# Kernel tuning notes

Hardware: AMD Instinct MI355X
Metric: run time of the kernel (lower is better)

## Reference

```python
import jax, jax.numpy as jnp
import numpy as np

N_NODES = 100000
N_EDGES = 3200000
N_FEAT = 64
HID = 64
GDIM = 32
N_CLASS = 2
NUM_GRAPHS = 16


def setup_inputs() -> dict:
    key = jax.random.key(0)
    ks = jax.random.split(key, 24)

    def w(k, fan_in, fan_out):
        return (jax.random.normal(k, (fan_in, fan_out), jnp.float32) / np.sqrt(fan_in)).astype(jnp.float32)

    inp = {
        'x': jax.random.normal(ks[0], (N_NODES, N_FEAT), jnp.float32),
        'edge_index': jax.random.randint(ks[1], (2, N_EDGES), 0, N_NODES, jnp.int32),
        'batch': jnp.sort(jax.random.randint(ks[2], (N_NODES,), 0, NUM_GRAPHS, jnp.int32)),
        # lin0: nr_features -> nhid0
        'lin0_w': w(ks[3], N_FEAT, HID), 'lin0_b': jnp.zeros((HID,), jnp.float32),
        # SAGEConv 1: lin_l (aggregated, with bias), lin_r (self, no bias)
        's1_lw': w(ks[4], HID, HID), 's1_lb': jnp.zeros((HID,), jnp.float32), 's1_rw': w(ks[5], HID, HID),
        # SAGEConv 2
        's2_lw': w(ks[6], HID, HID), 's2_lb': jnp.zeros((HID,), jnp.float32), 's2_rw': w(ks[7], HID, HID),
        # embedding heads
        'emb0_w': w(ks[8], HID, GDIM), 'emb0_b': jnp.zeros((GDIM,), jnp.float32),
        'emb1_w': w(ks[9], HID, GDIM), 'emb1_b': jnp.zeros((GDIM,), jnp.float32),
        'emb2_w': w(ks[10], HID, GDIM), 'emb2_b': jnp.zeros((GDIM,), jnp.float32),
        'merge_w': w(ks[11], 3 * GDIM, GDIM), 'merge_b': jnp.zeros((GDIM,), jnp.float32),
        # global attention pooling: gate_nn (GDIM->1), v_nn (GDIM->GDIM)
        'gate_w': w(ks[12], GDIM, 1), 'gate_b': jnp.zeros((1,), jnp.float32),
        'v_w': w(ks[13], GDIM, GDIM), 'v_b': jnp.zeros((GDIM,), jnp.float32),
        'out_w': w(ks[14], GDIM, N_CLASS), 'out_b': jnp.zeros((N_CLASS,), jnp.float32),
    }
    return inp


def _sage(x, src, dst, lw, lb, rw):
    # mean aggregation of source features at destination nodes
    deg = jax.ops.segment_sum(jnp.ones_like(src, jnp.float32), dst, num_segments=N_NODES)
    agg = jax.ops.segment_sum(x[src], dst, num_segments=N_NODES)
    mean = agg / jnp.maximum(deg, 1.0)[:, None]
    return mean @ lw + lb + x @ rw


def reference(x, edge_index, batch,
              lin0_w, lin0_b, s1_lw, s1_lb, s1_rw, s2_lw, s2_lb, s2_rw,
              emb0_w, emb0_b, emb1_w, emb1_b, emb2_w, emb2_b,
              merge_w, merge_b, gate_w, gate_b, v_w, v_b, out_w, out_b):
    src, dst = edge_index[0], edge_index[1]
    x0 = x @ lin0_w + lin0_b                       # [N, HID]
    x1 = _sage(x0, src, dst, s1_lw, s1_lb, s1_rw)  # [N, HID]
    x2 = _sage(x1, src, dst, s2_lw, s2_lb, s2_rw)  # [N, HID]
    # eval mode: dropout = identity
    e0 = jax.nn.relu(x0 @ emb0_w + emb0_b)
    e1 = jax.nn.relu(x1 @ emb1_w + emb1_b)
    e2 = jax.nn.relu(x2 @ emb2_w + emb2_b)
    xc = jax.nn.relu(jnp.concatenate([e0, e1, e2], axis=1) @ merge_w + merge_b)  # [N, GDIM]
    # global attention pooling with per-graph softmax
    g = (xc @ gate_w + gate_b)[:, 0]               # [N]
    v = xc @ v_w + v_b                             # [N, GDIM]
    m = jax.ops.segment_max(g, batch, num_segments=NUM_GRAPHS)
    e = jnp.exp(g - m[batch])
    d = jax.ops.segment_sum(e, batch, num_segments=NUM_GRAPHS)
    a = e / d[batch]
    pooled = jax.ops.segment_sum(a[:, None] * v, batch, num_segments=NUM_GRAPHS)  # [NG, GDIM]
    logits = pooled @ out_w + out_b                # [NG, 2]
    output1 = jax.nn.softmax(logits, axis=-1)
    output2 = logits
    return (output1, output2)
```

## Files before the change

kernel.cpp:

```cpp
#include <hip/hip_runtime.h>
#include <hip/hip_bf16.h>
#include <hip/hip_fp16.h>

#define N_NODES 100000
#define N_EDGES 3200000
#define HID 64
#define GDIM 32
#define NUM_GRAPHS 16
#define NB1 256
#define BSHIFT 9
#define B1 512

__device__ __forceinline__ unsigned fkey(float f) {
    unsigned u = __float_as_uint(f);
    return (u & 0x80000000u) ? ~u : (u | 0x80000000u);
}
__device__ __forceinline__ float funkey(unsigned k) {
    unsigned u = (k & 0x80000000u) ? (k ^ 0x80000000u) : ~k;
    return __uint_as_float(u);
}

struct half4 { __half2 lo, hi; };

__global__ __launch_bounds__(256) void hist1_kernel(const int* __restrict__ dst, int* __restrict__ h1, int E4) {
    __shared__ int h[NB1];
    int t = threadIdx.x, b = blockIdx.x;
    h[t] = 0;
    __syncthreads();
    for (int i = b * 256 + t; i < E4; i += B1 * 256) {
        int4 d = ((const int4*)dst)[i];
        atomicAdd(&h[d.x >> BSHIFT], 1);
        atomicAdd(&h[d.y >> BSHIFT], 1);
        atomicAdd(&h[d.z >> BSHIFT], 1);
        atomicAdd(&h[d.w >> BSHIFT], 1);
    }
    __syncthreads();
    h1[b * NB1 + t] = h[t];
}

__global__ __launch_bounds__(256) void scan1_kernel(const int* __restrict__ h1, int* __restrict__ off1,
                                                    int* __restrict__ bstart, int E) {
    __shared__ int ts[256];
    int t = threadIdx.x;
    int tot = 0;
    for (int k = 0; k < B1; k++) tot += h1[k * NB1 + t];
    ts[t] = tot;
    __syncthreads();
    for (int off = 1; off < 256; off <<= 1) {
        int v = (t >= off) ? ts[t - off] : 0;
        __syncthreads();
        ts[t] += v;
        __syncthreads();
    }
    int base = ts[t] - tot;
    bstart[t] = base;
    if (t == 255) bstart[256] = E;
    int run = base;
    for (int k = 0; k < B1; k++) { off1[k * NB1 + t] = run; run += h1[k * NB1 + t]; }
}

__global__ __launch_bounds__(256) void scatter1_kernel(const int* __restrict__ src, const int* __restrict__ dst,
                                                       const int* __restrict__ off1, int2* __restrict__ pairs, int E4) {
    __shared__ int cur[NB1];
    int t = threadIdx.x, b = blockIdx.x;
    cur[t] = off1[b * NB1 + t];
    __syncthreads();
    for (int i = b * 256 + t; i < E4; i += B1 * 256) {
        int4 d = ((const int4*)dst)[i];
        int4 s = ((const int4*)src)[i];
        int p0 = atomicAdd(&cur[d.x >> BSHIFT], 1);
        int p1 = atomicAdd(&cur[d.y >> BSHIFT], 1);
        int p2 = atomicAdd(&cur[d.z >> BSHIFT], 1);
        int p3 = atomicAdd(&cur[d.w >> BSHIFT], 1);
        pairs[p0] = make_int2(s.x, d.x);
        pairs[p1] = make_int2(s.y, d.y);
        pairs[p2] = make_int2(s.z, d.z);
        pairs[p3] = make_int2(s.w, d.w);
    }
}

__global__ __launch_bounds__(256) void bucket_csr_kernel(const int2* __restrict__ pairs, const int* __restrict__ bstart,
                                                         int* __restrict__ rowstart, int* __restrict__ csr,
                                                         int N, int E) {
    __shared__ int hist[512];
    __shared__ int ts[256];
    int b = blockIdx.x, t = threadIdx.x;
    int estart = bstart[b], eend = bstart[b + 1];
    hist[t] = 0; hist[t + 256] = 0;
    __syncthreads();
    for (int e = estart + t; e < eend; e += 256) {
        int2 pr = pairs[e];
        atomicAdd(&hist[pr.y & 511], 1);
    }
    __syncthreads();
    int a0 = hist[2 * t], a1 = hist[2 * t + 1];
    int s = a0 + a1;
    ts[t] = s;
    __syncthreads();
    for (int off = 1; off < 256; off <<= 1) {
        int v = (t >= off) ? ts[t - off] : 0;
        __syncthreads();
        ts[t] += v;
        __syncthreads();
    }
    int excl = ts[t] - s;
    __syncthreads();
    hist[2 * t]     = estart + excl;
    hist[2 * t + 1] = estart + excl + a0;
    int nb0 = b << BSHIFT;
    int i0 = nb0 + 2 * t, i1 = i0 + 1;
    if (i0 < N) rowstart[i0] = estart + excl;
    if (i1 < N) rowstart[i1] = estart + excl + a0;
    if (b == gridDim.x - 1 && t == 0) rowstart[N] = E;
    __syncthreads();
    for (int e = estart + t; e < eend; e += 256) {
        int2 pr = pairs[e];
        int p = atomicAdd(&hist[pr.y & 511], 1);
        csr[p] = pr.x;
    }
}

__global__ __launch_bounds__(256) void lin0_kernel(const float* __restrict__ x, const float* __restrict__ W,
                            const float* __restrict__ b, float* __restrict__ y, __half* __restrict__ yh, int N) {
    __shared__ __align__(16) float Wl[64 * 64];
    __shared__ float bl[64];
    int t = threadIdx.x;
    for (int i = t; i < 64 * 64; i += 256) Wl[i] = W[i];
    if (t < 64) bl[t] = b[t];
    __syncthreads();
    int row = blockIdx.x * 256 + t;
    if (row >= N) return;
    float acc[64];
#pragma unroll
    for (int j = 0; j < 64; j++) acc[j] = bl[j];
    const float4* xr = (const float4*)(x + (size_t)row * 64);
#pragma unroll
    for (int c = 0; c < 16; c++) {
        float4 xv = xr[c];
        float xs[4] = {xv.x, xv.y, xv.z, xv.w};
#pragma unroll
        for (int kk = 0; kk < 4; kk++) {
            int k = c * 4 + kk;
#pragma unroll
            for (int j4 = 0; j4 < 16; j4++) {
                float4 w = *(const float4*)&Wl[k * 64 + j4 * 4];
                acc[j4 * 4 + 0] += xs[kk] * w.x;
                acc[j4 * 4 + 1] += xs[kk] * w.y;
                acc[j4 * 4 + 2] += xs[kk] * w.z;
                acc[j4 * 4 + 3] += xs[kk] * w.w;
            }
        }
    }
    float4* yr = (float4*)(y + (size_t)row * 64);
#pragma unroll
    for (int c = 0; c < 16; c++)
        yr[c] = make_float4(acc[c * 4], acc[c * 4 + 1], acc[c * 4 + 2], acc[c * 4 + 3]);
    __half2* hr = (__half2*)(yh + (size_t)row * 64);
#pragma unroll
    for (int c = 0; c < 32; c++)
        hr[c] = __halves2half2(__float2half_rn(acc[c * 2]), __float2half_rn(acc[c * 2 + 1]));
}

__global__ __launch_bounds__(256) void agg_kernel(const __half* __restrict__ xh, const int* __restrict__ rowstart,
                           const int* __restrict__ csr, float* __restrict__ meanout, int N) {
    int wid = threadIdx.x >> 6, lane = threadIdx.x & 63;
    int node = blockIdx.x * 4 + wid;
    if (node >= N) return;
    int ro = rowstart[node], re = rowstart[node + 1];
    int g = lane >> 4, c4 = lane & 15;
    float4 acc = make_float4(0.f, 0.f, 0.f, 0.f);
    for (int base = ro; base < re; base += 64) {
        int rem = re - base;
        int idx = 0;
        if (lane < rem) idx = csr[base + lane];
        int kmax = rem < 64 ? rem : 64;
        for (int k = 0; k < kmax; k += 4) {
            int e = k + g;
            int s = __shfl(idx, e);
            if (e < kmax) {
                half4 hv = *(const half4*)(xh + (size_t)s * 64 + (c4 << 2));
                float2 f0 = __half22float2(hv.lo);
                float2 f1 = __half22float2(hv.hi);
                acc.x += f0.x; acc.y += f0.y; acc.z += f1.x; acc.w += f1.y;
            }
        }
    }
#pragma unroll
    for (int off = 16; off < 64; off <<= 1) {
        acc.x += __shfl_xor(acc.x, off);
        acc.y += __shfl_xor(acc.y, off);
        acc.z += __shfl_xor(acc.z, off);
        acc.w += __shfl_xor(acc.w, off);
    }
    int deg = re - ro;
    float inv = 1.0f / (float)(deg > 0 ? deg : 1);
    if (lane < 16) {
        ((float4*)(meanout + (size_t)node * 64))[c4] =
            make_float4(acc.x * inv, acc.y * inv, acc.z * inv, acc.w * inv);
    }
}

__global__ __launch_bounds__(256) void sage_kernel(const float* __restrict__ mean, const float* __restrict__ xin,
                            const float* __restrict__ lw, const float* __restrict__ lb,
                            const float* __restrict__ rw, float* __restrict__ xout,
                            __half* __restrict__ xhout, int N) {
    __shared__ __align__(16) float LW[64 * 64];
    __shared__ __align__(16) float RW[64 * 64];
    __shared__ float LB[64];
    int t = threadIdx.x;
    for (int i = t; i < 64 * 64; i += 256) { LW[i] = lw[i]; RW[i] = rw[i]; }
    if (t < 64) LB[t] = lb[t];
    __syncthreads();
    int row = blockIdx.x * 256 + t;
    if (row >= N) return;
    float acc[64];
#pragma unroll
    for (int j = 0; j < 64; j++) acc[j] = LB[j];
    const float4* mr = (const float4*)(mean + (size_t)row * 64);
    const float4* xr = (const float4*)(xin + (size_t)row * 64);
#pragma unroll
    for (int c = 0; c < 16; c++) {
        float4 xv = mr[c];
        float xs[4] = {xv.x, xv.y, xv.z, xv.w};
#pragma unroll
        for (int kk = 0; kk < 4; kk++) {
            int k = c * 4 + kk;
#pragma unroll
            for (int j4 = 0; j4 < 16; j4++) {
                float4 w = *(const float4*)&LW[k * 64 + j4 * 4];
                acc[j4 * 4 + 0] += xs[kk] * w.x;
                acc[j4 * 4 + 1] += xs[kk] * w.y;
                acc[j4 * 4 + 2] += xs[kk] * w.z;
                acc[j4 * 4 + 3] += xs[kk] * w.w;
            }
        }
    }
#pragma unroll
    for (int c = 0; c < 16; c++) {
        float4 xv = xr[c];
        float xs[4] = {xv.x, xv.y, xv.z, xv.w};
#pragma unroll
        for (int kk = 0; kk < 4; kk++) {
            int k = c * 4 + kk;
#pragma unroll
            for (int j4 = 0; j4 < 16; j4++) {
                float4 w = *(const float4*)&RW[k * 64 + j4 * 4];
                acc[j4 * 4 + 0] += xs[kk] * w.x;
                acc[j4 * 4 + 1] += xs[kk] * w.y;
                acc[j4 * 4 + 2] += xs[kk] * w.z;
                acc[j4 * 4 + 3] += xs[kk] * w.w;
            }
        }
    }
    float4* yr = (float4*)(xout + (size_t)row * 64);
#pragma unroll
    for (int c = 0; c < 16; c++)
        yr[c] = make_float4(acc[c * 4], acc[c * 4 + 1], acc[c * 4 + 2], acc[c * 4 + 3]);
    if (xhout) {
        __half2* hr = (__half2*)(xhout + (size_t)row * 64);
#pragma unroll
        for (int c = 0; c < 32; c++)
            hr[c] = __halves2half2(__float2half_rn(acc[c * 2]), __float2half_rn(acc[c * 2 + 1]));
    }
}

__global__ __launch_bounds__(256) void head_kernel(const float* __restrict__ x0, const float* __restrict__ x1,
                            const float* __restrict__ x2, const int* __restrict__ batch,
                            const float* __restrict__ e0w, const float* __restrict__ e0b,
                            const float* __restrict__ e1w, const float* __restrict__ e1b,
                            const float* __restrict__ e2w, const float* __restrict__ e2b,
                            const float* __restrict__ mw, const float* __restrict__ mb,
                            const float* __restrict__ gw, const float* __restrict__ gbp,
                            const float* __restrict__ vw, const float* __restrict__ vb,
                            float* __restrict__ gout, float* __restrict__ vout,
                            unsigned* __restrict__ mkey, int N) {
    __shared__ __align__(16) float EW[3 * 64 * 32];
    __shared__ __align__(16) float MW[96 * 32];
    __shared__ __align__(16) float VW[32 * 32];
    __shared__ float EB[96], MB[32], GW[32], VB[32];
    __shared__ float GB;
    __shared__ unsigned smax[16];
    int t = threadIdx.x;
    for (int i = t; i < 2048; i += 256) { EW[i] = e0w[i]; EW[2048 + i] = e1w[i]; EW[4096 + i] = e2w[i]; }
    for (int i = t; i < 3072; i += 256) MW[i] = mw[i];
    for (int i = t; i < 1024; i += 256) VW[i] = vw[i];
    if (t < 32) { EB[t] = e0b[t]; EB[32 + t] = e1b[t]; EB[64 + t] = e2b[t];
                  MB[t] = mb[t]; GW[t] = gw[t]; VB[t] = vb[t]; }
    if (t == 0) GB = gbp[0];
    if (t < 16) smax[t] = 0u;
    __syncthreads();
    int node = blockIdx.x * 256 + t;
    if (node < N) {
        float xc[32];
#pragma unroll
        for (int j = 0; j < 32; j++) xc[j] = MB[j];
        const float* px[3] = {x0 + (size_t)node * 64, x1 + (size_t)node * 64, x2 + (size_t)node * 64};
        for (int h = 0; h < 3; h++) {
            float e[32];
#pragma unroll
            for (int j = 0; j < 32; j++) e[j] = EB[h * 32 + j];
            const float4* xr = (const float4*)px[h];
#pragma unroll
            for (int c = 0; c < 16; c++) {
                float4 xv = xr[c];
                float xs[4] = {xv.x, xv.y, xv.z, xv.w};
#pragma unroll
                for (int kk = 0; kk < 4; kk++) {
                    int k = c * 4 + kk;
#pragma unroll
                    for (int j4 = 0; j4 < 8; j4++) {
                        float4 w = *(const float4*)&EW[h * 2048 + k * 32 + j4 * 4];
                        e[j4 * 4 + 0] += xs[kk] * w.x;
                        e[j4 * 4 + 1] += xs[kk] * w.y;
                        e[j4 * 4 + 2] += xs[kk] * w.z;
                        e[j4 * 4 + 3] += xs[kk] * w.w;
                    }
                }
            }
#pragma unroll
            for (int j = 0; j < 32; j++) e[j] = fmaxf(e[j], 0.f);
#pragma unroll
            for (int i = 0; i < 32; i++) {
#pragma unroll
                for (int j4 = 0; j4 < 8; j4++) {
                    float4 w = *(const float4*)&MW[(h * 32 + i) * 32 + j4 * 4];
                    xc[j4 * 4 + 0] += e[i] * w.x;
                    xc[j4 * 4 + 1] += e[i] * w.y;
                    xc[j4 * 4 + 2] += e[i] * w.z;
                    xc[j4 * 4 + 3] += e[i] * w.w;
                }
            }
        }
#pragma unroll
        for (int j = 0; j < 32; j++) xc[j] = fmaxf(xc[j], 0.f);
        float g = GB;
#pragma unroll
        for (int i = 0; i < 32; i++) g += xc[i] * GW[i];
        float vv[32];
#pragma unroll
        for (int j = 0; j < 32; j++) vv[j] = VB[j];
#pragma unroll
        for (int i = 0; i < 32; i++) {
#pragma unroll
            for (int j4 = 0; j4 < 8; j4++) {
                float4 w = *(const float4*)&VW[i * 32 + j4 * 4];
                vv[j4 * 4 + 0] += xc[i] * w.x;
                vv[j4 * 4 + 1] += xc[i] * w.y;
                vv[j4 * 4 + 2] += xc[i] * w.z;
                vv[j4 * 4 + 3] += xc[i] * w.w;
            }
        }
        gout[node] = g;
        float4* vr = (float4*)(vout + (size_t)node * 32);
#pragma unroll
        for (int c = 0; c < 8; c++)
            vr[c] = make_float4(vv[c * 4], vv[c * 4 + 1], vv[c * 4 + 2], vv[c * 4 + 3]);
        int b = batch[node];
        atomicMax(&smax[b], fkey(g));
    }
    __syncthreads();
    if (t < 16) atomicMax(&mkey[t], smax[t]);
}

__global__ __launch_bounds__(256) void pool_kernel(const float* __restrict__ g, const float* __restrict__ v,
                            const int* __restrict__ batch, const unsigned* __restrict__ mkey,
                            float* __restrict__ dsum, float* __restrict__ pooled, int N) {
    __shared__ float sd[16];
    __shared__ float sp[16 * 32];
    __shared__ float sm[16];
    int t = threadIdx.x;
    if (t < 16) { sd[t] = 0.f; sm[t] = funkey(mkey[t]); }
    for (int i = t; i < 512; i += 256) sp[i] = 0.f;
    __syncthreads();
    int node = blockIdx.x * 256 + t;
    if (node < N) {
        int b = batch[node];
        float e = __expf(g[node] - sm[b]);
        atomicAdd(&sd[b], e);
        const float4* vr = (const float4*)(v + (size_t)node * 32);
#pragma unroll
        for (int c = 0; c < 8; c++) {
            float4 vv = vr[c];
            atomicAdd(&sp[b * 32 + c * 4 + 0], e * vv.x);
            atomicAdd(&sp[b * 32 + c * 4 + 1], e * vv.y);
            atomicAdd(&sp[b * 32 + c * 4 + 2], e * vv.z);
            atomicAdd(&sp[b * 32 + c * 4 + 3], e * vv.w);
        }
    }
    __syncthreads();
    if (t < 16) atomicAdd(&dsum[t], sd[t]);
    for (int i = t; i < 512; i += 256) atomicAdd(&pooled[i], sp[i]);
}

__global__ __launch_bounds__(64) void final_kernel(const float* __restrict__ dsum, const float* __restrict__ pooled,
                             const float* __restrict__ ow, const float* __restrict__ ob,
                             float* __restrict__ out) {
    int t = threadIdx.x;
    if (t >= 16) return;
    float d = dsum[t];
    float l0 = ob[0], l1 = ob[1];
    for (int i = 0; i < 32; i++) {
        float p = pooled[t * 32 + i] / d;
        l0 += p * ow[i * 2 + 0];
        l1 += p * ow[i * 2 + 1];
    }
    float m = fmaxf(l0, l1);
    float e0 = __expf(l0 - m), e1 = __expf(l1 - m);
    float s = e0 + e1;
    out[t * 2 + 0] = e0 / s;
    out[t * 2 + 1] = e1 / s;
    out[32 + t * 2 + 0] = l0;
    out[32 + t * 2 + 1] = l1;
}

extern "C" void kernel_launch(void* const* d_in, const int* in_sizes, int n_in,
                              void* d_out, int out_size, void* d_ws, size_t ws_size,
                              hipStream_t stream) {
    const float* x       = (const float*)d_in[0];
    const int*   ei      = (const int*)d_in[1];
    const int*   batch   = (const int*)d_in[2];
    const float* lin0_w  = (const float*)d_in[3];
    const float* lin0_b  = (const float*)d_in[4];
    const float* s1_lw   = (const float*)d_in[5];
    const float* s1_lb   = (const float*)d_in[6];
    const float* s1_rw   = (const float*)d_in[7];
    const float* s2_lw   = (const float*)d_in[8];
    const float* s2_lb   = (const float*)d_in[9];
    const float* s2_rw   = (const float*)d_in[10];
    const float* e0w     = (const float*)d_in[11];
    const float* e0b     = (const float*)d_in[12];
    const float* e1w     = (const float*)d_in[13];
    const float* e1b     = (const float*)d_in[14];
    const float* e2w     = (const float*)d_in[15];
    const float* e2b     = (const float*)d_in[16];
    const float* mw      = (const float*)d_in[17];
    const float* mb      = (const float*)d_in[18];
    const float* gw      = (const float*)d_in[19];
    const float* gb      = (const float*)d_in[20];
    const float* vw      = (const float*)d_in[21];
    const float* vb      = (const float*)d_in[22];
    const float* ow      = (const float*)d_in[23];
    const float* ob      = (const float*)d_in[24];
    float* out = (float*)d_out;

    const int N = N_NODES, E = N_EDGES;
    const int* src = ei;
    const int* dst = ei + E;

    char* p = (char*)d_ws;
    auto carve = [&](size_t bytes) { char* r = p; p += (bytes + 255) & ~(size_t)255; return (void*)r; };
    float* x0      = (float*)carve((size_t)N * 64 * 4);
    float* x1      = (float*)carve((size_t)N * 64 * 4);
    float* x2      = (float*)carve((size_t)N * 64 * 4);
    __half* x0h    = (__half*)carve((size_t)N * 64 * 2);
    __half* x1h    = (__half*)carve((size_t)N * 64 * 2);
    float* meanb   = (float*)carve((size_t)N * 64 * 4);
    float* vbuf    = (float*)carve((size_t)N * 32 * 4);
    float* gbuf    = (float*)carve((size_t)N * 4);
    int*   csr     = (int*)carve((size_t)E * 4);
    int2*  pairs   = (int2*)carve((size_t)E * 8);
    int*   h1      = (int*)carve((size_t)B1 * NB1 * 4);
    int*   off1    = (int*)carve((size_t)B1 * NB1 * 4);
    int*   bstart  = (int*)carve((NB1 + 1) * 4);
    int*   rowstart= (int*)carve((size_t)(N + 1) * 4);
    unsigned* mkey = (unsigned*)carve(16 * 4);
    float* dsum    = (float*)carve(16 * 4);
    float* pooled  = (float*)carve(16 * 32 * 4);

    hipMemsetAsync(mkey, 0, 16 * 4, stream);
    hipMemsetAsync(dsum, 0, 16 * 4, stream);
    hipMemsetAsync(pooled, 0, 16 * 32 * 4, stream);

    const int E4 = E / 4;
    int nbl = (N + 255) / 256;
    int abl = (N + 3) / 4;
    const int NBUCK = (N + 511) >> BSHIFT;

    hist1_kernel<<<B1, 256, 0, stream>>>(dst, h1, E4);
    scan1_kernel<<<1, 256, 0, stream>>>(h1, off1, bstart, E);
    scatter1_kernel<<<B1, 256, 0, stream>>>(src, dst, off1, pairs, E4);
    bucket_csr_kernel<<<NBUCK, 256, 0, stream>>>(pairs, bstart, rowstart, csr, N, E);

    lin0_kernel<<<nbl, 256, 0, stream>>>(x, lin0_w, lin0_b, x0, x0h, N);

    agg_kernel<<<abl, 256, 0, stream>>>(x0h, rowstart, csr, meanb, N);
    sage_kernel<<<nbl, 256, 0, stream>>>(meanb, x0, s1_lw, s1_lb, s1_rw, x1, x1h, N);

    agg_kernel<<<abl, 256, 0, stream>>>(x1h, rowstart, csr, meanb, N);
    sage_kernel<<<nbl, 256, 0, stream>>>(meanb, x1, s2_lw, s2_lb, s2_rw, x2, (__half*)nullptr, N);

    head_kernel<<<nbl, 256, 0, stream>>>(x0, x1, x2, batch,
                                         e0w, e0b, e1w, e1b, e2w, e2b,
                                         mw, mb, gw, gb, vw, vb,
                                         gbuf, vbuf, mkey, N);

    pool_kernel<<<nbl, 256, 0, stream>>>(gbuf, vbuf, batch, mkey, dsum, pooled, N);

    final_kernel<<<1, 64, 0, stream>>>(dsum, pooled, ow, ob, out);
}
```

Baseline: 538.4 us.

## Pack edge pairs into one int and widen aggregation loads to 16 bytes

```diff
diff --git a/kernel.cpp b/kernel.cpp
--- a/kernel.cpp
+++ b/kernel.cpp
@@ -21,6 +21,7 @@
 }
 
 struct half4 { __half2 lo, hi; };
+struct __align__(16) half8 { __half2 a, b, c, d; };
 
 __global__ __launch_bounds__(256) void hist1_kernel(const int* __restrict__ dst, int* __restrict__ h1, int E4) {
     __shared__ int h[NB1];
@@ -60,7 +61,7 @@
 }
 
 __global__ __launch_bounds__(256) void scatter1_kernel(const int* __restrict__ src, const int* __restrict__ dst,
-                                                       const int* __restrict__ off1, int2* __restrict__ pairs, int E4) {
+                                                       const int* __restrict__ off1, int* __restrict__ pairs, int E4) {
     __shared__ int cur[NB1];
     int t = threadIdx.x, b = blockIdx.x;
     cur[t] = off1[b * NB1 + t];
@@ -72,14 +73,14 @@
         int p1 = atomicAdd(&cur[d.y >> BSHIFT], 1);
         int p2 = atomicAdd(&cur[d.z >> BSHIFT], 1);
         int p3 = atomicAdd(&cur[d.w >> BSHIFT], 1);
-        pairs[p0] = make_int2(s.x, d.x);
-        pairs[p1] = make_int2(s.y, d.y);
-        pairs[p2] = make_int2(s.z, d.z);
-        pairs[p3] = make_int2(s.w, d.w);
-    }
-}
-
-__global__ __launch_bounds__(256) void bucket_csr_kernel(const int2* __restrict__ pairs, const int* __restrict__ bstart,
+        pairs[p0] = (s.x << BSHIFT) | (d.x & 511);
+        pairs[p1] = (s.y << BSHIFT) | (d.y & 511);
+        pairs[p2] = (s.z << BSHIFT) | (d.z & 511);
+        pairs[p3] = (s.w << BSHIFT) | (d.w & 511);
+    }
+}
+
+__global__ __launch_bounds__(256) void bucket_csr_kernel(const int* __restrict__ pairs, const int* __restrict__ bstart,
                                                          int* __restrict__ rowstart, int* __restrict__ csr,
                                                          int N, int E) {
     __shared__ int hist[512];
@@ -89,8 +90,8 @@
     hist[t] = 0; hist[t + 256] = 0;
     __syncthreads();
     for (int e = estart + t; e < eend; e += 256) {
-        int2 pr = pairs[e];
-        atomicAdd(&hist[pr.y & 511], 1);
+        int pr = pairs[e];
+        atomicAdd(&hist[pr & 511], 1);
     }
     __syncthreads();
     int a0 = hist[2 * t], a1 = hist[2 * t + 1];
@@ -114,9 +115,9 @@
     if (b == gridDim.x - 1 && t == 0) rowstart[N] = E;
     __syncthreads();
     for (int e = estart + t; e < eend; e += 256) {
-        int2 pr = pairs[e];
-        int p = atomicAdd(&hist[pr.y & 511], 1);
-        csr[p] = pr.x;
+        int pr = pairs[e];
+        int p = atomicAdd(&hist[pr & 511], 1);
+        csr[p] = pr >> BSHIFT;
     }
 }
 
@@ -167,36 +168,40 @@
     int node = blockIdx.x * 4 + wid;
     if (node >= N) return;
     int ro = rowstart[node], re = rowstart[node + 1];
-    int g = lane >> 4, c4 = lane & 15;
-    float4 acc = make_float4(0.f, 0.f, 0.f, 0.f);
+    int g = lane >> 3, c8 = lane & 7;
+    float acc[8];
+#pragma unroll
+    for (int j = 0; j < 8; j++) acc[j] = 0.f;
     for (int base = ro; base < re; base += 64) {
         int rem = re - base;
         int idx = 0;
         if (lane < rem) idx = csr[base + lane];
         int kmax = rem < 64 ? rem : 64;
-        for (int k = 0; k < kmax; k += 4) {
+        for (int k = 0; k < kmax; k += 8) {
             int e = k + g;
             int s = __shfl(idx, e);
             if (e < kmax) {
-                half4 hv = *(const half4*)(xh + (size_t)s * 64 + (c4 << 2));
-                float2 f0 = __half22float2(hv.lo);
-                float2 f1 = __half22float2(hv.hi);
-                acc.x += f0.x; acc.y += f0.y; acc.z += f1.x; acc.w += f1.y;
-            }
-        }
-    }
-#pragma unroll
-    for (int off = 16; off < 64; off <<= 1) {
-        acc.x += __shfl_xor(acc.x, off);
-        acc.y += __shfl_xor(acc.y, off);
-        acc.z += __shfl_xor(acc.z, off);
-        acc.w += __shfl_xor(acc.w, off);
+                half8 hv = *(const half8*)(xh + (size_t)s * 64 + (c8 << 3));
+                float2 f0 = __half22float2(hv.a);
+                float2 f1 = __half22float2(hv.b);
+                float2 f2 = __half22float2(hv.c);
+                float2 f3 = __half22float2(hv.d);
+                acc[0] += f0.x; acc[1] += f0.y; acc[2] += f1.x; acc[3] += f1.y;
+                acc[4] += f2.x; acc[5] += f2.y; acc[6] += f3.x; acc[7] += f3.y;
+            }
+        }
+    }
+#pragma unroll
+    for (int off = 8; off < 64; off <<= 1) {
+#pragma unroll
+        for (int j = 0; j < 8; j++) acc[j] += __shfl_xor(acc[j], off);
     }
     int deg = re - ro;
     float inv = 1.0f / (float)(deg > 0 ? deg : 1);
-    if (lane < 16) {
-        ((float4*)(meanout + (size_t)node * 64))[c4] =
-            make_float4(acc.x * inv, acc.y * inv, acc.z * inv, acc.w * inv);
+    if (lane < 8) {
+        float4* mr = (float4*)(meanout + (size_t)node * 64 + (c8 << 3));
+        mr[0] = make_float4(acc[0] * inv, acc[1] * inv, acc[2] * inv, acc[3] * inv);
+        mr[1] = make_float4(acc[4] * inv, acc[5] * inv, acc[6] * inv, acc[7] * inv);
     }
 }
 
@@ -355,8 +360,7 @@
 #pragma unroll
         for (int c = 0; c < 8; c++)
             vr[c] = make_float4(vv[c * 4], vv[c * 4 + 1], vv[c * 4 + 2], vv[c * 4 + 3]);
-        int b = batch[node];
-        atomicMax(&smax[b], fkey(g));
+        atomicMax(&smax[batch[node]], fkey(g));
     }
     __syncthreads();
     if (t < 16) atomicMax(&mkey[t], smax[t]);
@@ -458,7 +462,7 @@
     float* vbuf    = (float*)carve((size_t)N * 32 * 4);
     float* gbuf    = (float*)carve((size_t)N * 4);
     int*   csr     = (int*)carve((size_t)E * 4);
-    int2*  pairs   = (int2*)carve((size_t)E * 8);
+    int*   pairs   = (int*)carve((size_t)E * 4);
     int*   h1      = (int*)carve((size_t)B1 * NB1 * 4);
     int*   off1    = (int*)carve((size_t)B1 * NB1 * 4);
     int*   bstart  = (int*)carve((NB1 + 1) * 4);
```

After: 508.6 us (median of 3 runs). 5.5% less time.
